# Kernel tuning notes

Hardware: AMD Instinct MI355X
Metric: run time of the kernel (lower is better)

The kernel has to match this reference:

```python
import jax, jax.numpy as jnp
import numpy as np

# PGA Cl(3,0,1) basis, ordering: 1, e0, e1, e2, e3, e01, e02, e03, e12, e13, e23, e012, e013, e023, e123, e0123
_BLADES = [(), (0,), (1,), (2,), (3,), (0, 1), (0, 2), (0, 3), (1, 2), (1, 3), (2, 3), (0, 1, 2), (0, 1, 3), (0, 2, 3), (1, 2, 3), (0, 1, 2, 3)]
_METRIC = [0.0, 1.0, 1.0, 1.0]  # e0^2 = 0 (degenerate), e1..e3 square to +1


def _blade_mul(a, b):
    coeffs = list(a) + list(b)
    sign = 1.0
    for _ in range(len(coeffs)):
        for q in range(len(coeffs) - 1):
            if coeffs[q] > coeffs[q + 1]:
                coeffs[q], coeffs[q + 1] = coeffs[q + 1], coeffs[q]
                sign = -sign
    out = []
    i = 0
    while i < len(coeffs):
        if i + 1 < len(coeffs) and coeffs[i] == coeffs[i + 1]:
            sign *= _METRIC[coeffs[i]]
            i += 2
        else:
            out.append(coeffs[i])
            i += 1
    return sign, tuple(out)


def _build_tables():
    idx = {b: i for i, b in enumerate(_BLADES)}
    C = np.zeros((16, 16, 16), np.float32)  # geometric-product Cayley table
    for i, a in enumerate(_BLADES):
        for j, b in enumerate(_BLADES):
            s, r = _blade_mul(a, b)
            if s != 0.0:
                C[i, j, idx[r]] += s
    grades = np.array([len(b) for b in _BLADES])
    # wedge = grade-raising part of the geometric product
    W = np.where(grades[:, None, None] + grades[None, :, None] == grades[None, None, :], C, 0.0).astype(np.float32)
    # dual via right complement: blade ^ complement = +e0123
    D = np.zeros((16, 16), np.float32)
    for i, b in enumerate(_BLADES):
        c = tuple(k for k in (0, 1, 2, 3) if k not in b)
        perm = list(b) + list(c)
        s = 1.0
        for _ in range(len(perm)):
            for q in range(len(perm) - 1):
                if perm[q] > perm[q + 1]:
                    perm[q], perm[q + 1] = perm[q + 1], perm[q]
                    s = -s
        D[idx[c], i] = s
    Dinv = np.linalg.inv(D).astype(np.float32)
    # join(x, y) = undual(dual(x) ^ dual(y)) as a single bilinear table
    J = np.einsum('ai,bj,abc,kc->ijk', D, D, W, Dinv).astype(np.float32)
    GM = (grades[None, :] == np.arange(5)[:, None]).astype(np.float32)  # (5, 16) grade masks
    return jnp.asarray(C), jnp.asarray(J), jnp.asarray(GM)


_C, _J, _GM = _build_tables()


def _gp(x, y):
    # geometric_product_batch: (..., 16) x (..., 16) -> (..., 16)
    return jnp.einsum('...i,...j,ijk->...k', x, y, _C)


def _join(x, y, ref):
    # equi_join_batch: pseudoscalar of reference gates the dual-wedge-undual join (E(3)-equivariance)
    return ref[..., 15:16] * jnp.einsum('...i,...j,ijk->...k', x, y, _J)


def _mv_linear(x, w, v, b):
    # MVLinear with in_channels = out_channels = 1: per-grade scaling + e0-product branch
    coef1 = (w.reshape(5)[:, None] * _GM).sum(0)          # (16,) per-component scale from 5 grade weights
    y1 = x * coef1
    y1 = y1.at[..., 0].add(b[0])                          # scalar bias on the grade-0 component
    e0x = jnp.einsum('...j,jk->...k', x, _C[1])           # left geometric product e0 * x
    coef2 = (v.reshape(4)[:, None] * _GM[:4]).sum(0)      # (16,) scale over grades 0..3 of e0*x
    return y1 + e0x * coef2


def setup_inputs() -> dict:
    key = jax.random.key(0)
    ks = jax.random.split(key, 7)
    B, N = 32, 8192
    return {
        'x': jax.random.normal(ks[0], (B, N, 16), jnp.float32),
        'w1': jax.random.normal(ks[1], (1, 1, 5), jnp.float32),
        'v1': jax.random.normal(ks[2], (1, 1, 4), jnp.float32),
        'b1': jnp.zeros((1,), jnp.float32),
        'w2g': jax.random.normal(ks[3], (1, 1, 5), jnp.float32),
        'v2g': jax.random.normal(ks[4], (1, 1, 4), jnp.float32),
        'b2g': jnp.zeros((1,), jnp.float32),
        'w2j': jax.random.normal(ks[5], (1, 1, 5), jnp.float32),
        'v2j': jax.random.normal(ks[6], (1, 1, 4), jnp.float32),
        'b2j': jnp.zeros((1,), jnp.float32),
    }


def reference(x, w1, v1, b1, w2g, v2g, b2g, w2j, v2j, b2j):
    x_proj = _mv_linear(x, w1, v1, b1)
    # MVGatedGelu: gate full multivector by exact gelu of its scalar component
    x_gated = jax.nn.gelu(x_proj[..., 0:1], approximate=False) * x_proj
    gp_part = _gp(x, x_gated)
    join_part = _join(x, x_gated, x)  # reference=None defaults to x
    # dropout is identity in eval mode
    return _mv_linear(gp_part, w2g, v2g, b2g) + _mv_linear(join_part, w2j, v2j, b2j)
```

## Files before the change

### kernel.cpp

```cpp
#include <hip/hip_runtime.h>
#include <math.h>

namespace ct {

constexpr int MASK[16] = {0, 1, 2, 4, 8, 3, 5, 9, 6, 10, 12, 7, 11, 13, 14, 15};
constexpr int IDX[16]  = {0, 1, 2, 5, 3, 6, 8, 11, 4, 7, 9, 12, 10, 13, 14, 15};
constexpr int GRADE[16] = {0, 1, 1, 1, 1, 2, 2, 2, 2, 2, 2, 3, 3, 3, 3, 4};

constexpr int popc(int v) { int c = 0; while (v) { c += v & 1; v >>= 1; } return c; }

constexpr int rs(int a, int b) {
    int s = 0;
    a >>= 1;
    while (a) { s += popc(a & b); a >>= 1; }
    return (s & 1) ? -1 : 1;
}

struct Tab { int sgn[16][16]; int idx[16][16]; };

constexpr Tab make_gp() {
    Tab t{};
    for (int i = 0; i < 16; ++i)
        for (int j = 0; j < 16; ++j) {
            int a = MASK[i], b = MASK[j];
            if (a & b & 1) { t.sgn[i][j] = 0; t.idx[i][j] = 0; }
            else           { t.sgn[i][j] = rs(a, b); t.idx[i][j] = IDX[a ^ b]; }
        }
    return t;
}

constexpr Tab make_jn() {
    Tab t{};
    for (int i = 0; i < 16; ++i)
        for (int j = 0; j < 16; ++j) {
            int a = MASK[i], b = MASK[j];
            int ca = 15 ^ a, cb = 15 ^ b;
            if (ca & cb) { t.sgn[i][j] = 0; t.idx[i][j] = 0; }
            else {
                int m = ca | cb;
                int p = 15 ^ m;
                t.sgn[i][j] = rs(a, ca) * rs(b, cb) * rs(ca, cb) * rs(p, m);
                t.idx[i][j] = IDX[p];
            }
        }
    return t;
}

constexpr Tab GP = make_gp();
constexpr Tab JN = make_jn();

}

__global__ __launch_bounds__(256) void mvffn_kernel(
    const float* __restrict__ x,
    const float* __restrict__ w1,  const float* __restrict__ v1,  const float* __restrict__ b1,
    const float* __restrict__ w2g, const float* __restrict__ v2g, const float* __restrict__ b2g,
    const float* __restrict__ w2j, const float* __restrict__ v2j, const float* __restrict__ b2j,
    float* __restrict__ out, int n)
{
    const int t = blockIdx.x * blockDim.x + threadIdx.x;
    if (t >= n) return;

    const float4* xv = reinterpret_cast<const float4*>(x) + (size_t)t * 4;
    float4 q0 = xv[0], q1 = xv[1], q2 = xv[2], q3 = xv[3];
    float X[16] = { q0.x, q0.y, q0.z, q0.w,  q1.x, q1.y, q1.z, q1.w,
                    q2.x, q2.y, q2.z, q2.w,  q3.x, q3.y, q3.z, q3.w };

    float W1[5], W2G[5], W2J[5], V1[4], V2G[4], V2J[4];
    #pragma unroll
    for (int i = 0; i < 5; ++i) { W1[i] = w1[i]; W2G[i] = w2g[i]; W2J[i] = w2j[i]; }
    #pragma unroll
    for (int i = 0; i < 4; ++i) { V1[i] = v1[i]; V2G[i] = v2g[i]; V2J[i] = v2j[i]; }
    const float B1 = b1[0], B2G = b2g[0], B2J = b2j[0];

    float xp[16];
    #pragma unroll
    for (int k = 0; k < 16; ++k) xp[k] = X[k] * W1[ct::GRADE[k]];
    xp[0]  += B1;
    xp[1]  += V1[1] * X[0];
    xp[5]  += V1[2] * X[2];
    xp[6]  += V1[2] * X[3];
    xp[7]  += V1[2] * X[4];
    xp[11] += V1[3] * X[8];
    xp[12] += V1[3] * X[9];
    xp[13] += V1[3] * X[10];

    const float s0 = xp[0];
    const float gate = 0.5f * s0 * (1.0f + erff(s0 * 0.70710678118654752f));
    float xg[16];
    #pragma unroll
    for (int k = 0; k < 16; ++k) xg[k] = gate * xp[k];

    float gp[16], jn[16];
    #pragma unroll
    for (int k = 0; k < 16; ++k) { gp[k] = 0.0f; jn[k] = 0.0f; }

    #pragma unroll
    for (int i = 0; i < 16; ++i) {
        #pragma unroll
        for (int j = 0; j < 16; ++j) {
            if (ct::GP.sgn[i][j] > 0)      gp[ct::GP.idx[i][j]] += X[i] * xg[j];
            else if (ct::GP.sgn[i][j] < 0) gp[ct::GP.idx[i][j]] -= X[i] * xg[j];
            if (ct::JN.sgn[i][j] > 0)      jn[ct::JN.idx[i][j]] += X[i] * xg[j];
            else if (ct::JN.sgn[i][j] < 0) jn[ct::JN.idx[i][j]] -= X[i] * xg[j];
        }
    }
    const float ps = X[15];
    #pragma unroll
    for (int k = 0; k < 16; ++k) jn[k] *= ps;

    float o[16];
    #pragma unroll
    for (int k = 0; k < 16; ++k)
        o[k] = gp[k] * W2G[ct::GRADE[k]] + jn[k] * W2J[ct::GRADE[k]];
    o[0]  += B2G + B2J;
    o[1]  += V2G[1] * gp[0]  + V2J[1] * jn[0];
    o[5]  += V2G[2] * gp[2]  + V2J[2] * jn[2];
    o[6]  += V2G[2] * gp[3]  + V2J[2] * jn[3];
    o[7]  += V2G[2] * gp[4]  + V2J[2] * jn[4];
    o[11] += V2G[3] * gp[8]  + V2J[3] * jn[8];
    o[12] += V2G[3] * gp[9]  + V2J[3] * jn[9];
    o[13] += V2G[3] * gp[10] + V2J[3] * jn[10];

    float4* ov = reinterpret_cast<float4*>(out) + (size_t)t * 4;
    ov[0] = make_float4(o[0],  o[1],  o[2],  o[3]);
    ov[1] = make_float4(o[4],  o[5],  o[6],  o[7]);
    ov[2] = make_float4(o[8],  o[9],  o[10], o[11]);
    ov[3] = make_float4(o[12], o[13], o[14], o[15]);
}

extern "C" void kernel_launch(void* const* d_in, const int* in_sizes, int n_in,
                              void* d_out, int out_size, void* d_ws, size_t ws_size,
                              hipStream_t stream) {
    const float* x   = (const float*)d_in[0];
    const float* w1  = (const float*)d_in[1];
    const float* v1  = (const float*)d_in[2];
    const float* b1  = (const float*)d_in[3];
    const float* w2g = (const float*)d_in[4];
    const float* v2g = (const float*)d_in[5];
    const float* b2g = (const float*)d_in[6];
    const float* w2j = (const float*)d_in[7];
    const float* v2j = (const float*)d_in[8];
    const float* b2j = (const float*)d_in[9];
    float* out = (float*)d_out;

    const int n = in_sizes[0] / 16;
    const int block = 256;
    const int grid = (n + block - 1) / block;
    mvffn_kernel<<<grid, block, 0, stream>>>(x, w1, v1, b1, w2g, v2g, b2g,
                                             w2j, v2j, b2j, out, n);
}
```

Measured before the change: 14.33 us.

## Stage multivector loads and stores through padded shared memory for coalescing

Global loads and stores of the 16-float multivectors now go through LDS, padded to 5 float4 per row. Each warp reads and writes contiguous float4s, and each thread then picks up its own multivector from LDS. This replaces per-thread strided 64-byte accesses. The pseudoscalar scaling of the join result is folded into the output weights, and launch bounds now request higher occupancy. The cost is extra LDS traffic, two barriers, and possible register pressure from the occupancy hint.

```diff
diff --git a/kernel.cpp b/kernel.cpp
--- a/kernel.cpp
+++ b/kernel.cpp
@@ -51,82 +51,123 @@
 
 }
 
-__global__ __launch_bounds__(256) void mvffn_kernel(
+__global__ __launch_bounds__(256, 4) void mvffn_kernel(
     const float* __restrict__ x,
     const float* __restrict__ w1,  const float* __restrict__ v1,  const float* __restrict__ b1,
     const float* __restrict__ w2g, const float* __restrict__ v2g, const float* __restrict__ b2g,
     const float* __restrict__ w2j, const float* __restrict__ v2j, const float* __restrict__ b2j,
     float* __restrict__ out, int n)
 {
-    const int t = blockIdx.x * blockDim.x + threadIdx.x;
-    if (t >= n) return;
+    const int tid = threadIdx.x;
+    const int mv0 = blockIdx.x * 256;
+    const bool full = (mv0 + 256 <= n);
+    const int mv = mv0 + tid;
 
-    const float4* xv = reinterpret_cast<const float4*>(x) + (size_t)t * 4;
-    float4 q0 = xv[0], q1 = xv[1], q2 = xv[2], q3 = xv[3];
-    float X[16] = { q0.x, q0.y, q0.z, q0.w,  q1.x, q1.y, q1.z, q1.w,
-                    q2.x, q2.y, q2.z, q2.w,  q3.x, q3.y, q3.z, q3.w };
+    __shared__ float4 sh[256 * 5];
 
-    float W1[5], W2G[5], W2J[5], V1[4], V2G[4], V2J[4];
-    #pragma unroll
-    for (int i = 0; i < 5; ++i) { W1[i] = w1[i]; W2G[i] = w2g[i]; W2J[i] = w2j[i]; }
-    #pragma unroll
-    for (int i = 0; i < 4; ++i) { V1[i] = v1[i]; V2G[i] = v2g[i]; V2J[i] = v2j[i]; }
-    const float B1 = b1[0], B2G = b2g[0], B2J = b2j[0];
-
-    float xp[16];
-    #pragma unroll
-    for (int k = 0; k < 16; ++k) xp[k] = X[k] * W1[ct::GRADE[k]];
-    xp[0]  += B1;
-    xp[1]  += V1[1] * X[0];
-    xp[5]  += V1[2] * X[2];
-    xp[6]  += V1[2] * X[3];
-    xp[7]  += V1[2] * X[4];
-    xp[11] += V1[3] * X[8];
-    xp[12] += V1[3] * X[9];
-    xp[13] += V1[3] * X[10];
-
-    const float s0 = xp[0];
-    const float gate = 0.5f * s0 * (1.0f + erff(s0 * 0.70710678118654752f));
-    float xg[16];
-    #pragma unroll
-    for (int k = 0; k < 16; ++k) xg[k] = gate * xp[k];
-
-    float gp[16], jn[16];
-    #pragma unroll
-    for (int k = 0; k < 16; ++k) { gp[k] = 0.0f; jn[k] = 0.0f; }
-
-    #pragma unroll
-    for (int i = 0; i < 16; ++i) {
+    float X[16];
+    if (full) {
+        const float4* gx = reinterpret_cast<const float4*>(x) + (size_t)mv0 * 4;
         #pragma unroll
-        for (int j = 0; j < 16; ++j) {
-            if (ct::GP.sgn[i][j] > 0)      gp[ct::GP.idx[i][j]] += X[i] * xg[j];
-            else if (ct::GP.sgn[i][j] < 0) gp[ct::GP.idx[i][j]] -= X[i] * xg[j];
-            if (ct::JN.sgn[i][j] > 0)      jn[ct::JN.idx[i][j]] += X[i] * xg[j];
-            else if (ct::JN.sgn[i][j] < 0) jn[ct::JN.idx[i][j]] -= X[i] * xg[j];
+        for (int k = 0; k < 4; ++k) {
+            const int u = tid + 256 * k;
+            sh[(u >> 2) * 5 + (u & 3)] = gx[u];
+        }
+        __syncthreads();
+        #pragma unroll
+        for (int j = 0; j < 4; ++j) {
+            float4 q = sh[tid * 5 + j];
+            X[4 * j + 0] = q.x; X[4 * j + 1] = q.y; X[4 * j + 2] = q.z; X[4 * j + 3] = q.w;
+        }
+        __syncthreads();
+    } else if (mv < n) {
+        const float4* xv = reinterpret_cast<const float4*>(x) + (size_t)mv * 4;
+        #pragma unroll
+        for (int j = 0; j < 4; ++j) {
+            float4 q = xv[j];
+            X[4 * j + 0] = q.x; X[4 * j + 1] = q.y; X[4 * j + 2] = q.z; X[4 * j + 3] = q.w;
         }
     }
-    const float ps = X[15];
-    #pragma unroll
-    for (int k = 0; k < 16; ++k) jn[k] *= ps;
 
     float o[16];
-    #pragma unroll
-    for (int k = 0; k < 16; ++k)
-        o[k] = gp[k] * W2G[ct::GRADE[k]] + jn[k] * W2J[ct::GRADE[k]];
-    o[0]  += B2G + B2J;
-    o[1]  += V2G[1] * gp[0]  + V2J[1] * jn[0];
-    o[5]  += V2G[2] * gp[2]  + V2J[2] * jn[2];
-    o[6]  += V2G[2] * gp[3]  + V2J[2] * jn[3];
-    o[7]  += V2G[2] * gp[4]  + V2J[2] * jn[4];
-    o[11] += V2G[3] * gp[8]  + V2J[3] * jn[8];
-    o[12] += V2G[3] * gp[9]  + V2J[3] * jn[9];
-    o[13] += V2G[3] * gp[10] + V2J[3] * jn[10];
+    if (full || mv < n) {
+        float W1[5], W2G[5], W2J[5], V1[4], V2G[4], V2J[4];
+        #pragma unroll
+        for (int i = 0; i < 5; ++i) { W1[i] = w1[i]; W2G[i] = w2g[i]; W2J[i] = w2j[i]; }
+        #pragma unroll
+        for (int i = 0; i < 4; ++i) { V1[i] = v1[i]; V2G[i] = v2g[i]; V2J[i] = v2j[i]; }
+        const float B1 = b1[0], B2G = b2g[0], B2J = b2j[0];
 
-    float4* ov = reinterpret_cast<float4*>(out) + (size_t)t * 4;
-    ov[0] = make_float4(o[0],  o[1],  o[2],  o[3]);
-    ov[1] = make_float4(o[4],  o[5],  o[6],  o[7]);
-    ov[2] = make_float4(o[8],  o[9],  o[10], o[11]);
-    ov[3] = make_float4(o[12], o[13], o[14], o[15]);
+        float xp[16];
+        #pragma unroll
+        for (int k = 0; k < 16; ++k) xp[k] = X[k] * W1[ct::GRADE[k]];
+        xp[0]  += B1;
+        xp[1]  += V1[1] * X[0];
+        xp[5]  += V1[2] * X[2];
+        xp[6]  += V1[2] * X[3];
+        xp[7]  += V1[2] * X[4];
+        xp[11] += V1[3] * X[8];
+        xp[12] += V1[3] * X[9];
+        xp[13] += V1[3] * X[10];
+
+        const float s0 = xp[0];
+        const float gate = 0.5f * s0 * (1.0f + erff(s0 * 0.70710678118654752f));
+        float xg[16];
+        #pragma unroll
+        for (int k = 0; k < 16; ++k) xg[k] = gate * xp[k];
+
+        float gp[16], jn[16];
+        #pragma unroll
+        for (int k = 0; k < 16; ++k) { gp[k] = 0.0f; jn[k] = 0.0f; }
+
+        #pragma unroll
+        for (int i = 0; i < 16; ++i) {
+            #pragma unroll
+            for (int j = 0; j < 16; ++j) {
+                if (ct::GP.sgn[i][j] > 0)      gp[ct::GP.idx[i][j]] += X[i] * xg[j];
+                else if (ct::GP.sgn[i][j] < 0) gp[ct::GP.idx[i][j]] -= X[i] * xg[j];
+                if (ct::JN.sgn[i][j] > 0)      jn[ct::JN.idx[i][j]] += X[i] * xg[j];
+                else if (ct::JN.sgn[i][j] < 0) jn[ct::JN.idx[i][j]] -= X[i] * xg[j];
+            }
+        }
+
+        const float ps = X[15];
+        float psW2J[5], psV2J[4];
+        #pragma unroll
+        for (int g = 0; g < 5; ++g) psW2J[g] = ps * W2J[g];
+        #pragma unroll
+        for (int g = 0; g < 4; ++g) psV2J[g] = ps * V2J[g];
+
+        #pragma unroll
+        for (int k = 0; k < 16; ++k)
+            o[k] = gp[k] * W2G[ct::GRADE[k]] + jn[k] * psW2J[ct::GRADE[k]];
+        o[0]  += B2G + B2J;
+        o[1]  += V2G[1] * gp[0]  + psV2J[1] * jn[0];
+        o[5]  += V2G[2] * gp[2]  + psV2J[2] * jn[2];
+        o[6]  += V2G[2] * gp[3]  + psV2J[2] * jn[3];
+        o[7]  += V2G[2] * gp[4]  + psV2J[2] * jn[4];
+        o[11] += V2G[3] * gp[8]  + psV2J[3] * jn[8];
+        o[12] += V2G[3] * gp[9]  + psV2J[3] * jn[9];
+        o[13] += V2G[3] * gp[10] + psV2J[3] * jn[10];
+    }
+
+    if (full) {
+        #pragma unroll
+        for (int j = 0; j < 4; ++j)
+            sh[tid * 5 + j] = make_float4(o[4 * j + 0], o[4 * j + 1], o[4 * j + 2], o[4 * j + 3]);
+        __syncthreads();
+        float4* gy = reinterpret_cast<float4*>(out) + (size_t)mv0 * 4;
+        #pragma unroll
+        for (int k = 0; k < 4; ++k) {
+            const int u = tid + 256 * k;
+            gy[u] = sh[(u >> 2) * 5 + (u & 3)];
+        }
+    } else if (mv < n) {
+        float4* ov = reinterpret_cast<float4*>(out) + (size_t)mv * 4;
+        #pragma unroll
+        for (int j = 0; j < 4; ++j)
+            ov[j] = make_float4(o[4 * j + 0], o[4 * j + 1], o[4 * j + 2], o[4 * j + 3]);
+    }
 }
 
 extern "C" void kernel_launch(void* const* d_in, const int* in_sizes, int n_in,
```

New measurement: 16.51 us. +15.2%, slower.

## Split each multivector across two lanes with shuffles, each computing half the outputs

Applied to the files above, without the earlier changes.

Each multivector is now handled by a pair of adjacent threads. Each thread loads 8 floats and exchanges them with its partner via __shfl_xor, so both lanes hold the full input. Each lane then computes only 8 of the 16 output components (geometric product and join) and writes them. This doubles the thread count and halves per-thread registers and arithmetic, in exchange for redundant projection/gelu work, shuffles, and divergent branches within each wavefront.

```diff
diff --git a/kernel.cpp b/kernel.cpp
--- a/kernel.cpp
+++ b/kernel.cpp
@@ -56,15 +56,15 @@
     const float* __restrict__ w1,  const float* __restrict__ v1,  const float* __restrict__ b1,
     const float* __restrict__ w2g, const float* __restrict__ v2g, const float* __restrict__ b2g,
     const float* __restrict__ w2j, const float* __restrict__ v2j, const float* __restrict__ b2j,
-    float* __restrict__ out, int n)
+    float* __restrict__ out, int n2)
 {
     const int t = blockIdx.x * blockDim.x + threadIdx.x;
-    if (t >= n) return;
+    if (t >= n2) return;
+    const bool podd = (t & 1);
 
-    const float4* xv = reinterpret_cast<const float4*>(x) + (size_t)t * 4;
-    float4 q0 = xv[0], q1 = xv[1], q2 = xv[2], q3 = xv[3];
-    float X[16] = { q0.x, q0.y, q0.z, q0.w,  q1.x, q1.y, q1.z, q1.w,
-                    q2.x, q2.y, q2.z, q2.w,  q3.x, q3.y, q3.z, q3.w };
+    const float4* x4 = reinterpret_cast<const float4*>(x);
+    float4 A = x4[2 * (size_t)t];
+    float4 B = x4[2 * (size_t)t + 1];
 
     float W1[5], W2G[5], W2J[5], V1[4], V2G[4], V2J[4];
     #pragma unroll
@@ -72,6 +72,23 @@
     #pragma unroll
     for (int i = 0; i < 4; ++i) { V1[i] = v1[i]; V2G[i] = v2g[i]; V2J[i] = v2j[i]; }
     const float B1 = b1[0], B2G = b2g[0], B2J = b2j[0];
+
+    float a0 = A.x, a1 = A.y, a2 = A.z, a3 = A.w;
+    float b0 = B.x, b1f = B.y, b2f = B.z, b3 = B.w;
+    float sa0 = __shfl_xor(a0, 1), sa1 = __shfl_xor(a1, 1),
+          sa2 = __shfl_xor(a2, 1), sa3 = __shfl_xor(a3, 1);
+    float sb0 = __shfl_xor(b0, 1), sb1 = __shfl_xor(b1f, 1),
+          sb2 = __shfl_xor(b2f, 1), sb3 = __shfl_xor(b3, 1);
+
+    float X[16];
+    X[0]  = podd ? sa0 : a0;   X[1]  = podd ? sa1 : a1;
+    X[2]  = podd ? sa2 : a2;   X[3]  = podd ? sa3 : a3;
+    X[4]  = podd ? sb0 : b0;   X[5]  = podd ? sb1 : b1f;
+    X[6]  = podd ? sb2 : b2f;  X[7]  = podd ? sb3 : b3;
+    X[8]  = podd ? a0 : sa0;   X[9]  = podd ? a1 : sa1;
+    X[10] = podd ? a2 : sa2;   X[11] = podd ? a3 : sa3;
+    X[12] = podd ? b0 : sb0;   X[13] = podd ? b1f : sb1;
+    X[14] = podd ? b2f : sb2;  X[15] = podd ? b3 : sb3;
 
     float xp[16];
     #pragma unroll
@@ -87,46 +104,71 @@
 
     const float s0 = xp[0];
     const float gate = 0.5f * s0 * (1.0f + erff(s0 * 0.70710678118654752f));
-    float xg[16];
     #pragma unroll
-    for (int k = 0; k < 16; ++k) xg[k] = gate * xp[k];
+    for (int k = 0; k < 16; ++k) xp[k] *= gate;
 
-    float gp[16], jn[16];
-    #pragma unroll
-    for (int k = 0; k < 16; ++k) { gp[k] = 0.0f; jn[k] = 0.0f; }
+    const float ps = X[15];
 
-    #pragma unroll
-    for (int i = 0; i < 16; ++i) {
+    float o[8];
+    if (!podd) {
+        float c1 = 0.f, c5 = 0.f, c6 = 0.f, c7 = 0.f;
         #pragma unroll
-        for (int j = 0; j < 16; ++j) {
-            if (ct::GP.sgn[i][j] > 0)      gp[ct::GP.idx[i][j]] += X[i] * xg[j];
-            else if (ct::GP.sgn[i][j] < 0) gp[ct::GP.idx[i][j]] -= X[i] * xg[j];
-            if (ct::JN.sgn[i][j] > 0)      jn[ct::JN.idx[i][j]] += X[i] * xg[j];
-            else if (ct::JN.sgn[i][j] < 0) jn[ct::JN.idx[i][j]] -= X[i] * xg[j];
+        for (int r = 0; r < 8; ++r) {
+            const int k = r;
+            float g = 0.f, h = 0.f;
+            #pragma unroll
+            for (int i = 0; i < 16; ++i) {
+                #pragma unroll
+                for (int j = 0; j < 16; ++j) {
+                    if (ct::GP.sgn[i][j] > 0 && ct::GP.idx[i][j] == k)      g += X[i] * xp[j];
+                    else if (ct::GP.sgn[i][j] < 0 && ct::GP.idx[i][j] == k) g -= X[i] * xp[j];
+                    if (ct::JN.sgn[i][j] > 0 && ct::JN.idx[i][j] == k)      h += X[i] * xp[j];
+                    else if (ct::JN.sgn[i][j] < 0 && ct::JN.idx[i][j] == k) h -= X[i] * xp[j];
+                }
+            }
+            h *= ps;
+            float val = g * W2G[ct::GRADE[k]] + h * W2J[ct::GRADE[k]];
+            if (k == 0) { val += B2G + B2J; c1 = V2G[1] * g + V2J[1] * h; }
+            if (k == 2) { c5 = V2G[2] * g + V2J[2] * h; }
+            if (k == 3) { c6 = V2G[2] * g + V2J[2] * h; }
+            if (k == 4) { c7 = V2G[2] * g + V2J[2] * h; }
+            if (k == 1) val += c1;
+            if (k == 5) val += c5;
+            if (k == 6) val += c6;
+            if (k == 7) val += c7;
+            o[r] = val;
+        }
+    } else {
+        float c11 = 0.f, c12 = 0.f, c13 = 0.f;
+        #pragma unroll
+        for (int r = 0; r < 8; ++r) {
+            const int k = 8 + r;
+            float g = 0.f, h = 0.f;
+            #pragma unroll
+            for (int i = 0; i < 16; ++i) {
+                #pragma unroll
+                for (int j = 0; j < 16; ++j) {
+                    if (ct::GP.sgn[i][j] > 0 && ct::GP.idx[i][j] == k)      g += X[i] * xp[j];
+                    else if (ct::GP.sgn[i][j] < 0 && ct::GP.idx[i][j] == k) g -= X[i] * xp[j];
+                    if (ct::JN.sgn[i][j] > 0 && ct::JN.idx[i][j] == k)      h += X[i] * xp[j];
+                    else if (ct::JN.sgn[i][j] < 0 && ct::JN.idx[i][j] == k) h -= X[i] * xp[j];
+                }
+            }
+            h *= ps;
+            float val = g * W2G[ct::GRADE[k]] + h * W2J[ct::GRADE[k]];
+            if (k == 8)  { c11 = V2G[3] * g + V2J[3] * h; }
+            if (k == 9)  { c12 = V2G[3] * g + V2J[3] * h; }
+            if (k == 10) { c13 = V2G[3] * g + V2J[3] * h; }
+            if (k == 11) val += c11;
+            if (k == 12) val += c12;
+            if (k == 13) val += c13;
+            o[r] = val;
         }
     }
-    const float ps = X[15];
-    #pragma unroll
-    for (int k = 0; k < 16; ++k) jn[k] *= ps;
 
-    float o[16];
-    #pragma unroll
-    for (int k = 0; k < 16; ++k)
-        o[k] = gp[k] * W2G[ct::GRADE[k]] + jn[k] * W2J[ct::GRADE[k]];
-    o[0]  += B2G + B2J;
-    o[1]  += V2G[1] * gp[0]  + V2J[1] * jn[0];
-    o[5]  += V2G[2] * gp[2]  + V2J[2] * jn[2];
-    o[6]  += V2G[2] * gp[3]  + V2J[2] * jn[3];
-    o[7]  += V2G[2] * gp[4]  + V2J[2] * jn[4];
-    o[11] += V2G[3] * gp[8]  + V2J[3] * jn[8];
-    o[12] += V2G[3] * gp[9]  + V2J[3] * jn[9];
-    o[13] += V2G[3] * gp[10] + V2J[3] * jn[10];
-
-    float4* ov = reinterpret_cast<float4*>(out) + (size_t)t * 4;
-    ov[0] = make_float4(o[0],  o[1],  o[2],  o[3]);
-    ov[1] = make_float4(o[4],  o[5],  o[6],  o[7]);
-    ov[2] = make_float4(o[8],  o[9],  o[10], o[11]);
-    ov[3] = make_float4(o[12], o[13], o[14], o[15]);
+    float4* out4 = reinterpret_cast<float4*>(out);
+    out4[2 * (size_t)t]     = make_float4(o[0], o[1], o[2], o[3]);
+    out4[2 * (size_t)t + 1] = make_float4(o[4], o[5], o[6], o[7]);
 }
 
 extern "C" void kernel_launch(void* const* d_in, const int* in_sizes, int n_in,
@@ -144,9 +186,10 @@
     const float* b2j = (const float*)d_in[9];
     float* out = (float*)d_out;
 
-    const int n = in_sizes[0] / 16;
+    const int n  = in_sizes[0] / 16;
+    const int n2 = 2 * n;
     const int block = 256;
-    const int grid = (n + block - 1) / block;
+    const int grid = (n2 + block - 1) / block;
     mvffn_kernel<<<grid, block, 0, stream>>>(x, w1, v1, b1, w2g, v2g, b2g,
-                                             w2j, v2j, b2j, out, n);
+                                             w2j, v2j, b2j, out, n2);
 }
```

Result: slower. 17.78 us (+24.0%).

## Process two multivectors per thread and compute outputs component by component

Applied to the files above, without the earlier changes.

Each thread now loads both multivectors up front and processes them in turn, halving the grid. The bilinear products are reorganised so each output component's gp and join sums are computed and consumed immediately, instead of keeping two 16-float accumulator arrays live. The aim is more memory-level parallelism per thread and lower register pressure. Holding the second input's 16 floats live during the first computation can raise register use. Having fewer threads may also reduce latency hiding on this memory-bound kernel.

```diff
diff --git a/kernel.cpp b/kernel.cpp
--- a/kernel.cpp
+++ b/kernel.cpp
@@ -51,6 +51,66 @@
 
 }
 
+struct Params {
+    float W1[5], W2G[5], W2J[5], V1[4], V2G[4], V2J[4];
+    float B1, B2G, B2J;
+};
+
+__device__ __forceinline__ void mv_ffn_one(const float X[16], const Params& P, float o[16]) {
+    float xp[16];
+    #pragma unroll
+    for (int k = 0; k < 16; ++k) xp[k] = X[k] * P.W1[ct::GRADE[k]];
+    xp[0]  += P.B1;
+    xp[1]  += P.V1[1] * X[0];
+    xp[5]  += P.V1[2] * X[2];
+    xp[6]  += P.V1[2] * X[3];
+    xp[7]  += P.V1[2] * X[4];
+    xp[11] += P.V1[3] * X[8];
+    xp[12] += P.V1[3] * X[9];
+    xp[13] += P.V1[3] * X[10];
+
+    const float s0 = xp[0];
+    const float gate = 0.5f * s0 * (1.0f + erff(s0 * 0.70710678118654752f));
+    #pragma unroll
+    for (int k = 0; k < 16; ++k) xp[k] *= gate;
+
+    const float ps = X[15];
+
+    float c1 = 0.f, c5 = 0.f, c6 = 0.f, c7 = 0.f, c11 = 0.f, c12 = 0.f, c13 = 0.f;
+    #pragma unroll
+    for (int k = 0; k < 16; ++k) {
+        float g = 0.f, h = 0.f;
+        #pragma unroll
+        for (int i = 0; i < 16; ++i) {
+            #pragma unroll
+            for (int j = 0; j < 16; ++j) {
+                if (ct::GP.sgn[i][j] > 0 && ct::GP.idx[i][j] == k)      g += X[i] * xp[j];
+                else if (ct::GP.sgn[i][j] < 0 && ct::GP.idx[i][j] == k) g -= X[i] * xp[j];
+                if (ct::JN.sgn[i][j] > 0 && ct::JN.idx[i][j] == k)      h += X[i] * xp[j];
+                else if (ct::JN.sgn[i][j] < 0 && ct::JN.idx[i][j] == k) h -= X[i] * xp[j];
+            }
+        }
+        h *= ps;
+
+        float val = g * P.W2G[ct::GRADE[k]] + h * P.W2J[ct::GRADE[k]];
+        if (k == 0)  { val += P.B2G + P.B2J; c1 = P.V2G[1] * g + P.V2J[1] * h; }
+        if (k == 2)  { c5  = P.V2G[2] * g + P.V2J[2] * h; }
+        if (k == 3)  { c6  = P.V2G[2] * g + P.V2J[2] * h; }
+        if (k == 4)  { c7  = P.V2G[2] * g + P.V2J[2] * h; }
+        if (k == 8)  { c11 = P.V2G[3] * g + P.V2J[3] * h; }
+        if (k == 9)  { c12 = P.V2G[3] * g + P.V2J[3] * h; }
+        if (k == 10) { c13 = P.V2G[3] * g + P.V2J[3] * h; }
+        if (k == 1)  val += c1;
+        if (k == 5)  val += c5;
+        if (k == 6)  val += c6;
+        if (k == 7)  val += c7;
+        if (k == 11) val += c11;
+        if (k == 12) val += c12;
+        if (k == 13) val += c13;
+        o[k] = val;
+    }
+}
+
 __global__ __launch_bounds__(256) void mvffn_kernel(
     const float* __restrict__ x,
     const float* __restrict__ w1,  const float* __restrict__ v1,  const float* __restrict__ b1,
@@ -59,74 +119,54 @@
     float* __restrict__ out, int n)
 {
     const int t = blockIdx.x * blockDim.x + threadIdx.x;
-    if (t >= n) return;
+    const int m0 = 2 * t;
+    const int m1 = 2 * t + 1;
+    if (m0 >= n) return;
+    const bool has1 = (m1 < n);
 
-    const float4* xv = reinterpret_cast<const float4*>(x) + (size_t)t * 4;
-    float4 q0 = xv[0], q1 = xv[1], q2 = xv[2], q3 = xv[3];
-    float X[16] = { q0.x, q0.y, q0.z, q0.w,  q1.x, q1.y, q1.z, q1.w,
-                    q2.x, q2.y, q2.z, q2.w,  q3.x, q3.y, q3.z, q3.w };
+    const float4* x4 = reinterpret_cast<const float4*>(x);
+    float4 A0 = x4[4 * (size_t)m0 + 0];
+    float4 A1 = x4[4 * (size_t)m0 + 1];
+    float4 A2 = x4[4 * (size_t)m0 + 2];
+    float4 A3 = x4[4 * (size_t)m0 + 3];
+    float4 B0, B1v, B2, B3;
+    if (has1) {
+        B0  = x4[4 * (size_t)m1 + 0];
+        B1v = x4[4 * (size_t)m1 + 1];
+        B2  = x4[4 * (size_t)m1 + 2];
+        B3  = x4[4 * (size_t)m1 + 3];
+    }
 
-    float W1[5], W2G[5], W2J[5], V1[4], V2G[4], V2J[4];
+    Params P;
     #pragma unroll
-    for (int i = 0; i < 5; ++i) { W1[i] = w1[i]; W2G[i] = w2g[i]; W2J[i] = w2j[i]; }
+    for (int i = 0; i < 5; ++i) { P.W1[i] = w1[i]; P.W2G[i] = w2g[i]; P.W2J[i] = w2j[i]; }
     #pragma unroll
-    for (int i = 0; i < 4; ++i) { V1[i] = v1[i]; V2G[i] = v2g[i]; V2J[i] = v2j[i]; }
-    const float B1 = b1[0], B2G = b2g[0], B2J = b2j[0];
+    for (int i = 0; i < 4; ++i) { P.V1[i] = v1[i]; P.V2G[i] = v2g[i]; P.V2J[i] = v2j[i]; }
+    P.B1 = b1[0]; P.B2G = b2g[0]; P.B2J = b2j[0];
 
-    float xp[16];
-    #pragma unroll
-    for (int k = 0; k < 16; ++k) xp[k] = X[k] * W1[ct::GRADE[k]];
-    xp[0]  += B1;
-    xp[1]  += V1[1] * X[0];
-    xp[5]  += V1[2] * X[2];
-    xp[6]  += V1[2] * X[3];
-    xp[7]  += V1[2] * X[4];
-    xp[11] += V1[3] * X[8];
-    xp[12] += V1[3] * X[9];
-    xp[13] += V1[3] * X[10];
+    float4* out4 = reinterpret_cast<float4*>(out);
 
-    const float s0 = xp[0];
-    const float gate = 0.5f * s0 * (1.0f + erff(s0 * 0.70710678118654752f));
-    float xg[16];
-    #pragma unroll
-    for (int k = 0; k < 16; ++k) xg[k] = gate * xp[k];
+    {
+        float X[16] = { A0.x, A0.y, A0.z, A0.w,  A1.x, A1.y, A1.z, A1.w,
+                        A2.x, A2.y, A2.z, A2.w,  A3.x, A3.y, A3.z, A3.w };
+        float o[16];
+        mv_ffn_one(X, P, o);
+        out4[4 * (size_t)m0 + 0] = make_float4(o[0],  o[1],  o[2],  o[3]);
+        out4[4 * (size_t)m0 + 1] = make_float4(o[4],  o[5],  o[6],  o[7]);
+        out4[4 * (size_t)m0 + 2] = make_float4(o[8],  o[9],  o[10], o[11]);
+        out4[4 * (size_t)m0 + 3] = make_float4(o[12], o[13], o[14], o[15]);
+    }
 
-    float gp[16], jn[16];
-    #pragma unroll
-    for (int k = 0; k < 16; ++k) { gp[k] = 0.0f; jn[k] = 0.0f; }
-
-    #pragma unroll
-    for (int i = 0; i < 16; ++i) {
-        #pragma unroll
-        for (int j = 0; j < 16; ++j) {
-            if (ct::GP.sgn[i][j] > 0)      gp[ct::GP.idx[i][j]] += X[i] * xg[j];
-            else if (ct::GP.sgn[i][j] < 0) gp[ct::GP.idx[i][j]] -= X[i] * xg[j];
-            if (ct::JN.sgn[i][j] > 0)      jn[ct::JN.idx[i][j]] += X[i] * xg[j];
-            else if (ct::JN.sgn[i][j] < 0) jn[ct::JN.idx[i][j]] -= X[i] * xg[j];
-        }
+    if (has1) {
+        float X[16] = { B0.x,  B0.y,  B0.z,  B0.w,   B1v.x, B1v.y, B1v.z, B1v.w,
+                        B2.x,  B2.y,  B2.z,  B2.w,   B3.x,  B3.y,  B3.z,  B3.w };
+        float o[16];
+        mv_ffn_one(X, P, o);
+        out4[4 * (size_t)m1 + 0] = make_float4(o[0],  o[1],  o[2],  o[3]);
+        out4[4 * (size_t)m1 + 1] = make_float4(o[4],  o[5],  o[6],  o[7]);
+        out4[4 * (size_t)m1 + 2] = make_float4(o[8],  o[9],  o[10], o[11]);
+        out4[4 * (size_t)m1 + 3] = make_float4(o[12], o[13], o[14], o[15]);
     }
-    const float ps = X[15];
-    #pragma unroll
-    for (int k = 0; k < 16; ++k) jn[k] *= ps;
-
-    float o[16];
-    #pragma unroll
-    for (int k = 0; k < 16; ++k)
-        o[k] = gp[k] * W2G[ct::GRADE[k]] + jn[k] * W2J[ct::GRADE[k]];
-    o[0]  += B2G + B2J;
-    o[1]  += V2G[1] * gp[0]  + V2J[1] * jn[0];
-    o[5]  += V2G[2] * gp[2]  + V2J[2] * jn[2];
-    o[6]  += V2G[2] * gp[3]  + V2J[2] * jn[3];
-    o[7]  += V2G[2] * gp[4]  + V2J[2] * jn[4];
-    o[11] += V2G[3] * gp[8]  + V2J[3] * jn[8];
-    o[12] += V2G[3] * gp[9]  + V2J[3] * jn[9];
-    o[13] += V2G[3] * gp[10] + V2J[3] * jn[10];
-
-    float4* ov = reinterpret_cast<float4*>(out) + (size_t)t * 4;
-    ov[0] = make_float4(o[0],  o[1],  o[2],  o[3]);
-    ov[1] = make_float4(o[4],  o[5],  o[6],  o[7]);
-    ov[2] = make_float4(o[8],  o[9],  o[10], o[11]);
-    ov[3] = make_float4(o[12], o[13], o[14], o[15]);
 }
 
 extern "C" void kernel_launch(void* const* d_in, const int* in_sizes, int n_in,
@@ -144,9 +184,10 @@
     const float* b2j = (const float*)d_in[9];
     float* out = (float*)d_out;
 
-    const int n = in_sizes[0] / 16;
+    const int n  = in_sizes[0] / 16;
+    const int nt = (n + 1) / 2;
     const int block = 256;
-    const int grid = (n + block - 1) / block;
+    const int grid = (nt + block - 1) / block;
     mvffn_kernel<<<grid, block, 0, stream>>>(x, w1, v1, b1, w2g, v2g, b2g,
                                              w2j, v2j, b2j, out, n);
 }
```

After: 15.17 us. +5.8%, slower.
